# Kernel tuning notes

Measured on AMD Instinct MI355X. Metric: run time of the kernel, lower is better.

Reference implementation:

```python
import jax, jax.numpy as jnp
import numpy as np
from jax import lax

B, CIN, H, W = 8, 64, 128, 128
COUT, K, STRIDE, PAD = 128, 3, 1, 1
NLEV = 256  # 2**activation_bits == 2**weight_bits


def setup_inputs() -> dict:
    key = jax.random.key(0)
    kx, kw = jax.random.split(key)
    x = jax.random.uniform(kx, (B, CIN, H, W), dtype=jnp.float32)
    weight = jax.random.normal(kw, (COUT, CIN, K, K), dtype=jnp.float32)
    bias = jnp.zeros((COUT,), dtype=jnp.float32)
    return {"x": x, "weight": weight, "bias": bias}


def _lut_table(weight):
    # quantized weights in [0, 255], integer-valued
    qw = jnp.clip(jnp.round(weight * (NLEV - 1)), 0, NLEV - 1).astype(jnp.int32)
    iv = jnp.arange(NLEV, dtype=jnp.int32)
    # emulate torch .to(int16) wraparound (qw*i can exceed 32767)
    lut = (qw[..., None] * iv).astype(jnp.int16)          # [O, C, K, K, 256]
    # the original sums pcilt over its (c,p,q) dims for EVERY patch entry;
    # precollapse those dims: T[i, o] = sum_{c,p,q} lut[o,c,p,q,i]
    T = lut.astype(jnp.int32).sum(axis=(1, 2, 3))          # [O, 256]
    return T.T                                             # [256, O]


def reference(x, weight, bias):
    T = _lut_table(weight)                                 # [256, COUT]
    xq = jnp.clip(jnp.round(x * (NLEV - 1)), 0, NLEV - 1).astype(jnp.int32)
    xp = jnp.pad(xq, ((0, 0), (0, 0), (PAD, PAD), (PAD, PAD)))  # zero-pad; T[:,0]=0 matches
    xc = jnp.moveaxis(xp, 1, 0)                            # [CIN, B, Hp, Wp]

    # accumulate per-pixel channel sum of LUT rows: A[b,h,w,o] = sum_c T[x[b,c,h,w], o]
    A0 = jnp.zeros((xp.shape[0], xp.shape[2], xp.shape[3], COUT), dtype=jnp.int32)

    def body(acc, ch):
        return acc + T[ch], None

    A, _ = lax.scan(body, A0, xc)                          # [B, Hp, Wp, COUT]

    # k x k sliding-window sum over spatial dims = sum over all patch entries
    out = lax.reduce_window(A.astype(jnp.float32), 0.0, lax.add,
                            (1, K, K, 1), (1, STRIDE, STRIDE, 1), 'VALID')
    out = jnp.moveaxis(out, 3, 1) + bias[None, :, None, None]  # [B, COUT, OH, OW]
    return out
```

## Files before the change

### kernel.cpp

```cpp
#include <hip/hip_runtime.h>

#define CIN   64
#define HW    128
#define COUT  128
#define TH    8
#define TW    32
#define NITER 12
#define NTHR  512
#define HSTR  144
#define SLOT  (34 * HSTR)
#define H3SL  (32 * HSTR)

#define HM_OFF    0
#define H3_OFF    19584
#define SX_OFF    38016
#define SXP_OFF   39296
#define SX9_OFF   42560
#define LDS_BYTES 42880

typedef int v4i __attribute__((ext_vector_type(4)));

__device__ __forceinline__ void wg_barrier() {
  asm volatile("s_waitcnt lgkmcnt(0)\n\ts_barrier" ::: "memory");
}

__device__ __forceinline__ int quad_sum(int v) {
  v += __builtin_amdgcn_mov_dpp(v, 0xB1, 0xF, 0xF, true);
  v += __builtin_amdgcn_mov_dpp(v, 0x4E, 0xF, 0xF, true);
  return v;
}

__global__ __launch_bounds__(512)
void build_tables(const float* __restrict__ weight, int* __restrict__ W_tab,
                  char* __restrict__ Kt_g) {
  __shared__ int qw_s[576];
  __shared__ int red_s[144];
  const int o = blockIdx.x;
  const int t = threadIdx.x;
  for (int j = t; j < 576; j += 512) {
    float w = weight[o * 576 + j];
    int q = (int)rintf(w * 255.f);
    qw_s[j] = q < 0 ? 0 : (q > 255 ? 255 : q);
  }
  __syncthreads();
  const int v = t >> 2, part = t & 3;
  const int i = 128 + v;
  int cnt = 0;
  const int j0 = part * 144;
  for (int j = j0; j < j0 + 144; ++j) cnt += (qw_s[j] * i) > 32767 ? 1 : 0;
  cnt = quad_sum(cnt);
  if (part == 0) Kt_g[o * 128 + v] = (char)(cnt - 128);
  if (t < 144)
    red_s[t] = qw_s[t * 4] + qw_s[t * 4 + 1] + qw_s[t * 4 + 2] + qw_s[t * 4 + 3];
  __syncthreads();
  if (t == 0) {
    int s = 0;
    for (int kk = 0; kk < 144; ++kk) s += red_s[kk];
    W_tab[o] = s;
  }
}

__global__ __launch_bounds__(NTHR, 4)
void pcilt_main(const float* __restrict__ x, const float* __restrict__ bias,
                const int* __restrict__ W_tab, const char* __restrict__ Kt_g,
                float* __restrict__ out) {
  __shared__ uint4 ldsv[LDS_BYTES / 16];
  char* ldsb = (char*)ldsv;
  unsigned char* HmB = (unsigned char*)(ldsb + HM_OFF);
  unsigned char* H3B = (unsigned char*)(ldsb + H3_OFF);
  unsigned char* KtB = (unsigned char*)(ldsb + H3_OFF);
  int* Sx  = (int*)(ldsb + SX_OFF);
  int* Sxp = (int*)(ldsb + SXP_OFF);
  int* Sx9 = (int*)(ldsb + SX9_OFF);

  const int t   = (int)threadIdx.x;
  const int bid = (int)blockIdx.x;
  const int b  = bid & 7;
  const int k  = bid >> 3;
  const int h0 = (k >> 2) * TH;
  const int w0 = (k & 3) * TW;

  for (int i = t; i < 4096; i += NTHR)
    ((unsigned int*)KtB)[i] = ((const unsigned int*)Kt_g)[i];
  {
    const uint4 z4 = make_uint4(0, 0, 0, 0);
    for (int i = t; i < SLOT / 16; i += NTHR) ((uint4*)HmB)[i] = z4;
  }

  const int l    = t & 15;
  const int slot = t >> 4;
  const int wv   = t >> 6;
  const int kq   = (t >> 4) & 3;
  const int Mt   = wv >> 2;
  const int Nh   = wv & 3;
  const int o0   = Nh * 32 + l;

  const float wfo0 = (float)W_tab[o0],      bio0 = bias[o0];
  const float wfo1 = (float)W_tab[o0 + 16], bio1 = bias[o0 + 16];

  float pf0[4], pf1[4];
  int qv[2][8];
  const float* xb = x + ((size_t)b * CIN + l * 4) * (HW * HW);
  const size_t cs = (size_t)HW * HW;

#define ISSUE(rn)                                                              \
  {                                                                            \
    const int iy  = h0 + (rn)-1;                                               \
    const int iyc = iy < 0 ? 0 : (iy > 127 ? 127 : iy);                        \
    const bool rok = (iy >= 0) && (iy < HW);                                   \
    int ix = w0 + slot - 1;                                                    \
    int ixc = ix < 0 ? 0 : (ix > 127 ? 127 : ix);                              \
    bool ok = rok && (ix >= 0) && (ix < HW);                                   \
    const float* xp = xb + (size_t)iyc * HW + ixc;                             \
    float v0 = xp[0], v1 = xp[cs], v2 = xp[2 * cs], v3 = xp[3 * cs];           \
    pf0[0] = ok ? v0 : 0.f; pf0[1] = ok ? v1 : 0.f;                            \
    pf0[2] = ok ? v2 : 0.f; pf0[3] = ok ? v3 : 0.f;                            \
    if (slot >= 30) {                                                          \
      ix = w0 + slot + 1;                                    \
      ixc = ix > 127 ? 127 : ix;                                               \
      ok = rok && (ix < HW);                                                   \
      const float* xq = xb + (size_t)iyc * HW + ixc;                           \
      float u0 = xq[0], u1 = xq[cs], u2 = xq[2 * cs], u3 = xq[3 * cs];         \
      pf1[0] = ok ? u0 : 0.f; pf1[1] = ok ? u1 : 0.f;                          \
      pf1[2] = ok ? u2 : 0.f; pf1[3] = ok ? u3 : 0.f;                          \
    }                                                                          \
  }

#define QUANT4(pf, qn, base, px, sxpb)                                         \
  {                                                                            \
    int q;                                                                     \
    q = (int)rintf((pf)[0] * 255.f); (qn)[(base)+0] = q < 0 ? 0 : (q > 255 ? 255 : q); \
    q = (int)rintf((pf)[1] * 255.f); (qn)[(base)+1] = q < 0 ? 0 : (q > 255 ? 255 : q); \
    q = (int)rintf((pf)[2] * 255.f); (qn)[(base)+2] = q < 0 ? 0 : (q > 255 ? 255 : q); \
    q = (int)rintf((pf)[3] * 255.f); (qn)[(base)+3] = q < 0 ? 0 : (q > 255 ? 255 : q); \
    int pk = (((qn)[(base)+0] > 128) + ((qn)[(base)+1] > 128) +                \
              ((qn)[(base)+2] > 128) + ((qn)[(base)+3] > 128));                \
    pk = (pk << 20) + (qn)[(base)+0] + (qn)[(base)+1] + (qn)[(base)+2] + (qn)[(base)+3]; \
    pk = quad_sum(pk);                                                         \
    if ((l & 3) == 0) Sxp[(sxpb) + (px)*12 + (l >> 2)] = pk;                   \
  }

#define HIST4(q0, q1, q2, q3, px, Hc)                                          \
  {                                                                            \
    unsigned char* hp = (Hc) + (px)*HSTR;                                      \
    if ((q0) > 128) { int v = (q0) - 128; atomicAdd((unsigned int*)(hp + ((v >> 2) << 2)), 1u << ((v & 3) * 8)); } \
    if ((q1) > 128) { int v = (q1) - 128; atomicAdd((unsigned int*)(hp + ((v >> 2) << 2)), 1u << ((v & 3) * 8)); } \
    if ((q2) > 128) { int v = (q2) - 128; atomicAdd((unsigned int*)(hp + ((v >> 2) << 2)), 1u << ((v & 3) * 8)); } \
    if ((q3) > 128) { int v = (q3) - 128; atomicAdd((unsigned int*)(hp + ((v >> 2) << 2)), 1u << ((v & 3) * 8)); } \
  }

  ISSUE(0);
  wg_barrier();

  v4i bfr[2][2];
#pragma unroll
  for (int nt = 0; nt < 2; ++nt)
#pragma unroll
    for (int k64 = 0; k64 < 2; ++k64)
      bfr[nt][k64] = *(const v4i*)(KtB + (o0 + nt * 16) * 128 + k64 * 64 + kq * 16);

  QUANT4(pf0, qv[0], 0, slot, 0);
  if (slot >= 30) QUANT4(pf1, qv[0], 4, slot + 2, 0);
  ISSUE(1);
  wg_barrier();

#pragma unroll
  for (int r = 0; r < NITER; ++r) {
    if (r <= 9) {
      unsigned char* Hc = HmB + (r & 3) * SLOT;
      const int* qc = qv[r & 1];
      HIST4(qc[0], qc[1], qc[2], qc[3], slot, Hc);
      if (slot >= 30) HIST4(qc[4], qc[5], qc[6], qc[7], slot + 2, Hc);
    }
    if (r >= 1 && r <= 10 && t < 256) {
      const int px = t & 31, ch = (t >> 5) * 16;
      const unsigned char* hs = HmB + ((r - 1) & 3) * SLOT + px * HSTR + ch;
      const uint4 a0 = *(const uint4*)hs;
      const uint4 a1 = *(const uint4*)(hs + HSTR);
      const uint4 a2 = *(const uint4*)(hs + 2 * HSTR);
      uint4 s;
      s.x = a0.x + a1.x + a2.x; s.y = a0.y + a1.y + a2.y;
      s.z = a0.z + a1.z + a2.z; s.w = a0.w + a1.w + a2.w;
      *(uint4*)(H3B + ((r - 1) & 3) * H3SL + px * HSTR + ch) = s;
    }
    if (r >= 4) {
      v4i acc0 = (v4i){0, 0, 0, 0}, acc1 = (v4i){0, 0, 0, 0};
#pragma unroll
      for (int st = 0; st < 3; ++st) {
        const unsigned char* Hs = H3B + ((r - 4 + st) & 3) * H3SL +
                                  (Mt * 16 + l) * HSTR + kq * 16;
#pragma unroll
        for (int k64 = 0; k64 < 2; ++k64) {
          const v4i a = *(const v4i*)(Hs + k64 * 64);
          acc0 = __builtin_amdgcn_mfma_i32_16x16x64_i8(a, bfr[0][k64], acc0, 0, 0, 0);
          acc1 = __builtin_amdgcn_mfma_i32_16x16x64_i8(a, bfr[1][k64], acc1, 0, 0, 0);
        }
      }
      const int j = r - 4, h = h0 + j, px0 = Mt * 16 + kq * 4;
      const v4i s9 = *(const v4i*)&Sx9[(j & 1) * 40 + px0];
      float4 u0, u1;
#pragma unroll
      for (int rg = 0; rg < 4; ++rg) {
        const int sx = s9[rg] & 0xFFFFF;
        const int sh = s9[rg] >> 20;
        ((float*)&u0)[rg] = (float)sx * wfo0 - 65536.f * (float)(acc0[rg] + (sh << 7)) + bio0;
        ((float*)&u1)[rg] = (float)sx * wfo1 - 65536.f * (float)(acc1[rg] + (sh << 7)) + bio1;
      }
      float* op = out + (((size_t)b * COUT + o0) * HW + h) * HW + w0 + px0;
      *(float4*)op = u0;
      *(float4*)(op + 16 * (size_t)(HW * HW)) = u1;
    }
    if (r <= 9 && wv == 7) {
      const int L = t - 448;
      if (L < 34) {
        const v4i sq = *(const v4i*)&Sxp[(r & 1) * 408 + L * 12];
        Sx[(r & 7) * 40 + L] = sq.x + sq.y + sq.z + sq.w;
      }
    }
    if (r >= 3 && r <= 10 && wv == 6 && (t & 32)) {
      const int L = t - 416;
      int v9 = 0;
#pragma unroll
      for (int q = 0; q < 3; ++q) {
        const int sl = ((r - 3 + q) & 7) * 40;
        v9 += Sx[sl + L] + Sx[sl + L + 1] + Sx[sl + L + 2];
      }
      Sx9[((r - 3) & 1) * 40 + L] = v9;
    }
    if (r <= 8 && wv >= 4 && wv < 6) {
      uint4* Hn = (uint4*)(HmB + ((r + 1) & 3) * SLOT);
      const uint4 z4 = make_uint4(0, 0, 0, 0);
      for (int i2 = t - 256; i2 < SLOT / 16; i2 += 128) Hn[i2] = z4;
    }
    if (r <= 8) {
      const int sxpb = ((r + 1) & 1) * 408;
      int* qn = qv[(r + 1) & 1];
      QUANT4(pf0, qn, 0, slot, sxpb);
      if (slot >= 30) QUANT4(pf1, qn, 4, slot + 2, sxpb);
    }
    if (r <= 7) ISSUE(r + 2);

    wg_barrier();
  }
}

extern "C" void kernel_launch(void* const* d_in, const int* in_sizes, int n_in,
                              void* d_out, int out_size, void* d_ws, size_t ws_size,
                              hipStream_t stream) {
  const float* x      = (const float*)d_in[0];
  const float* weight = (const float*)d_in[1];
  const float* bias   = (const float*)d_in[2];
  float* out = (float*)d_out;

  int*  W_tab = (int*)d_ws;
  char* Kt_g  = (char*)d_ws + 512;

  build_tables<<<128, 512, 0, stream>>>(weight, W_tab, Kt_g);

  pcilt_main<<<512, NTHR, 0, stream>>>(x, bias, W_tab, Kt_g, out);
}
```

Baseline: 44.34 us.

## Preload and quantize all input rows upfront, packing bytes and computing row sums once

Replaces the per-iteration prefetch/quantize pipeline with a single upfront loop that loads all 10 input rows, quantizes them into packed byte registers, and computes per-pixel channel sums with a 16-lane DPP reduction written straight to LDS. The 3x3 window sums are then computed once at iteration zero instead of by dedicated waves inside each pipeline step. This is meant to issue all global loads at once for more memory-level parallelism and to drop per-iteration quantization and Sx bookkeeping. The cost is more live registers (20 packed dwords plus the load burst) and a serialized load phase before histogramming starts, with no overlap against compute.

```diff
diff --git a/kernel.cpp b/kernel.cpp
--- a/kernel.cpp
+++ b/kernel.cpp
@@ -13,10 +13,9 @@
 
 #define HM_OFF    0
 #define H3_OFF    19584
-#define SX_OFF    38016
-#define SXP_OFF   39296
-#define SX9_OFF   42560
-#define LDS_BYTES 42880
+#define SXR_OFF   38016
+#define SX9_OFF   39616
+#define LDS_BYTES 40896
 
 typedef int v4i __attribute__((ext_vector_type(4)));
 
@@ -27,6 +26,12 @@
 __device__ __forceinline__ int quad_sum(int v) {
   v += __builtin_amdgcn_mov_dpp(v, 0xB1, 0xF, 0xF, true);
   v += __builtin_amdgcn_mov_dpp(v, 0x4E, 0xF, 0xF, true);
+  return v;
+}
+__device__ __forceinline__ int row16_sum(int v) {
+  v = quad_sum(v);
+  v += __builtin_amdgcn_mov_dpp(v, 0x114, 0xF, 0xF, true);
+  v += __builtin_amdgcn_mov_dpp(v, 0x118, 0xF, 0xF, true);
   return v;
 }
 
@@ -69,8 +74,7 @@
   unsigned char* HmB = (unsigned char*)(ldsb + HM_OFF);
   unsigned char* H3B = (unsigned char*)(ldsb + H3_OFF);
   unsigned char* KtB = (unsigned char*)(ldsb + H3_OFF);
-  int* Sx  = (int*)(ldsb + SX_OFF);
-  int* Sxp = (int*)(ldsb + SXP_OFF);
+  int* SxR = (int*)(ldsb + SXR_OFF);
   int* Sx9 = (int*)(ldsb + SX9_OFF);
 
   const int t   = (int)threadIdx.x;
@@ -98,79 +102,92 @@
   const float wfo0 = (float)W_tab[o0],      bio0 = bias[o0];
   const float wfo1 = (float)W_tab[o0 + 16], bio1 = bias[o0 + 16];
 
-  float pf0[4], pf1[4];
-  int qv[2][8];
-  const float* xb = x + ((size_t)b * CIN + l * 4) * (HW * HW);
-  const size_t cs = (size_t)HW * HW;
-
-#define ISSUE(rn)                                                              \
-  {                                                                            \
-    const int iy  = h0 + (rn)-1;                                               \
-    const int iyc = iy < 0 ? 0 : (iy > 127 ? 127 : iy);                        \
-    const bool rok = (iy >= 0) && (iy < HW);                                   \
-    int ix = w0 + slot - 1;                                                    \
-    int ixc = ix < 0 ? 0 : (ix > 127 ? 127 : ix);                              \
-    bool ok = rok && (ix >= 0) && (ix < HW);                                   \
-    const float* xp = xb + (size_t)iyc * HW + ixc;                             \
-    float v0 = xp[0], v1 = xp[cs], v2 = xp[2 * cs], v3 = xp[3 * cs];           \
-    pf0[0] = ok ? v0 : 0.f; pf0[1] = ok ? v1 : 0.f;                            \
-    pf0[2] = ok ? v2 : 0.f; pf0[3] = ok ? v3 : 0.f;                            \
-    if (slot >= 30) {                                                          \
-      ix = w0 + slot + 1;                                    \
-      ixc = ix > 127 ? 127 : ix;                                               \
-      ok = rok && (ix < HW);                                                   \
-      const float* xq = xb + (size_t)iyc * HW + ixc;                           \
-      float u0 = xq[0], u1 = xq[cs], u2 = xq[2 * cs], u3 = xq[3 * cs];         \
-      pf1[0] = ok ? u0 : 0.f; pf1[1] = ok ? u1 : 0.f;                          \
-      pf1[2] = ok ? u2 : 0.f; pf1[3] = ok ? u3 : 0.f;                          \
-    }                                                                          \
-  }
-
-#define QUANT4(pf, qn, base, px, sxpb)                                         \
-  {                                                                            \
-    int q;                                                                     \
-    q = (int)rintf((pf)[0] * 255.f); (qn)[(base)+0] = q < 0 ? 0 : (q > 255 ? 255 : q); \
-    q = (int)rintf((pf)[1] * 255.f); (qn)[(base)+1] = q < 0 ? 0 : (q > 255 ? 255 : q); \
-    q = (int)rintf((pf)[2] * 255.f); (qn)[(base)+2] = q < 0 ? 0 : (q > 255 ? 255 : q); \
-    q = (int)rintf((pf)[3] * 255.f); (qn)[(base)+3] = q < 0 ? 0 : (q > 255 ? 255 : q); \
-    int pk = (((qn)[(base)+0] > 128) + ((qn)[(base)+1] > 128) +                \
-              ((qn)[(base)+2] > 128) + ((qn)[(base)+3] > 128));                \
-    pk = (pk << 20) + (qn)[(base)+0] + (qn)[(base)+1] + (qn)[(base)+2] + (qn)[(base)+3]; \
-    pk = quad_sum(pk);                                                         \
-    if ((l & 3) == 0) Sxp[(sxpb) + (px)*12 + (l >> 2)] = pk;                   \
-  }
-
-#define HIST4(q0, q1, q2, q3, px, Hc)                                          \
+  wg_barrier();
+
+  v4i bfr[2][2];
+#pragma unroll
+  for (int nt = 0; nt < 2; ++nt)
+#pragma unroll
+    for (int k64 = 0; k64 < 2; ++k64)
+      bfr[nt][k64] = *(const v4i*)(KtB + (o0 + nt * 16) * 128 + k64 * 64 + kq * 16);
+
+  unsigned int qd[10], qd2[10];
+  {
+    const float* xb = x + ((size_t)b * CIN + l * 4) * (HW * HW);
+    const size_t cs = (size_t)HW * HW;
+    const int ix0 = w0 + slot - 1;
+    const int ix0c = ix0 < 0 ? 0 : (ix0 > 127 ? 127 : ix0);
+    const bool wok0 = (ix0 >= 0) && (ix0 < HW);
+    const int ix1 = w0 + slot + 1;
+    const int ix1c = ix1 > 127 ? 127 : ix1;
+    const bool wok1 = ix1 < HW;
+    const bool dual = slot >= 30;
+#pragma unroll
+    for (int row = 0; row < 10; ++row) {
+      const int iy = h0 + row - 1;
+      const int iyc = iy < 0 ? 0 : (iy > 127 ? 127 : iy);
+      const bool rok = (iy >= 0) && (iy < HW);
+      {
+        const float* xp = xb + (size_t)iyc * HW + ix0c;
+        const bool ok = rok && wok0;
+        float f0 = xp[0], f1 = xp[cs], f2 = xp[2 * cs], f3 = xp[3 * cs];
+        f0 = ok ? f0 : 0.f; f1 = ok ? f1 : 0.f; f2 = ok ? f2 : 0.f; f3 = ok ? f3 : 0.f;
+        int q0 = (int)rintf(f0 * 255.f); q0 = q0 < 0 ? 0 : (q0 > 255 ? 255 : q0);
+        int q1 = (int)rintf(f1 * 255.f); q1 = q1 < 0 ? 0 : (q1 > 255 ? 255 : q1);
+        int q2 = (int)rintf(f2 * 255.f); q2 = q2 < 0 ? 0 : (q2 > 255 ? 255 : q2);
+        int q3 = (int)rintf(f3 * 255.f); q3 = q3 < 0 ? 0 : (q3 > 255 ? 255 : q3);
+        qd[row] = (unsigned)q0 | ((unsigned)q1 << 8) | ((unsigned)q2 << 16) | ((unsigned)q3 << 24);
+        int pk = (((q0 > 128) + (q1 > 128) + (q2 > 128) + (q3 > 128)) << 20) +
+                 (q0 + q1 + q2 + q3);
+        pk = row16_sum(pk);
+        if (l == 15) SxR[row * 40 + slot] = pk;
+      }
+      {
+        const float* xp = xb + (size_t)iyc * HW + ix1c;
+        const bool ok = dual && rok && wok1;
+        float f0 = ok ? xp[0] : 0.f, f1 = ok ? xp[cs] : 0.f;
+        float f2 = ok ? xp[2 * cs] : 0.f, f3 = ok ? xp[3 * cs] : 0.f;
+        int q0 = (int)rintf(f0 * 255.f); q0 = q0 < 0 ? 0 : (q0 > 255 ? 255 : q0);
+        int q1 = (int)rintf(f1 * 255.f); q1 = q1 < 0 ? 0 : (q1 > 255 ? 255 : q1);
+        int q2 = (int)rintf(f2 * 255.f); q2 = q2 < 0 ? 0 : (q2 > 255 ? 255 : q2);
+        int q3 = (int)rintf(f3 * 255.f); q3 = q3 < 0 ? 0 : (q3 > 255 ? 255 : q3);
+        qd2[row] = (unsigned)q0 | ((unsigned)q1 << 8) | ((unsigned)q2 << 16) | ((unsigned)q3 << 24);
+        int pk = (((q0 > 128) + (q1 > 128) + (q2 > 128) + (q3 > 128)) << 20) +
+                 (q0 + q1 + q2 + q3);
+        pk = row16_sum(pk);
+        if (dual && l == 15) SxR[row * 40 + slot + 2] = pk;
+      }
+    }
+  }
+  wg_barrier();
+
+#define HISTD(dw, px, Hc)                                                      \
   {                                                                            \
     unsigned char* hp = (Hc) + (px)*HSTR;                                      \
-    if ((q0) > 128) { int v = (q0) - 128; atomicAdd((unsigned int*)(hp + ((v >> 2) << 2)), 1u << ((v & 3) * 8)); } \
-    if ((q1) > 128) { int v = (q1) - 128; atomicAdd((unsigned int*)(hp + ((v >> 2) << 2)), 1u << ((v & 3) * 8)); } \
-    if ((q2) > 128) { int v = (q2) - 128; atomicAdd((unsigned int*)(hp + ((v >> 2) << 2)), 1u << ((v & 3) * 8)); } \
-    if ((q3) > 128) { int v = (q3) - 128; atomicAdd((unsigned int*)(hp + ((v >> 2) << 2)), 1u << ((v & 3) * 8)); } \
-  }
-
-  ISSUE(0);
-  wg_barrier();
-
-  v4i bfr[2][2];
-#pragma unroll
-  for (int nt = 0; nt < 2; ++nt)
-#pragma unroll
-    for (int k64 = 0; k64 < 2; ++k64)
-      bfr[nt][k64] = *(const v4i*)(KtB + (o0 + nt * 16) * 128 + k64 * 64 + kq * 16);
-
-  QUANT4(pf0, qv[0], 0, slot, 0);
-  if (slot >= 30) QUANT4(pf1, qv[0], 4, slot + 2, 0);
-  ISSUE(1);
-  wg_barrier();
+    const unsigned b0 = (dw) & 255u, b1 = ((dw) >> 8) & 255u;                  \
+    const unsigned b2 = ((dw) >> 16) & 255u, b3 = (dw) >> 24;                  \
+    if (b0 > 128u) { unsigned v = b0 - 128u; atomicAdd((unsigned*)(hp + ((v >> 2) << 2)), 1u << ((v & 3) * 8)); } \
+    if (b1 > 128u) { unsigned v = b1 - 128u; atomicAdd((unsigned*)(hp + ((v >> 2) << 2)), 1u << ((v & 3) * 8)); } \
+    if (b2 > 128u) { unsigned v = b2 - 128u; atomicAdd((unsigned*)(hp + ((v >> 2) << 2)), 1u << ((v & 3) * 8)); } \
+    if (b3 > 128u) { unsigned v = b3 - 128u; atomicAdd((unsigned*)(hp + ((v >> 2) << 2)), 1u << ((v & 3) * 8)); } \
+  }
 
 #pragma unroll
   for (int r = 0; r < NITER; ++r) {
     if (r <= 9) {
       unsigned char* Hc = HmB + (r & 3) * SLOT;
-      const int* qc = qv[r & 1];
-      HIST4(qc[0], qc[1], qc[2], qc[3], slot, Hc);
-      if (slot >= 30) HIST4(qc[4], qc[5], qc[6], qc[7], slot + 2, Hc);
+      HISTD(qd[r], slot, Hc);
+      if (slot >= 30) HISTD(qd2[r], slot + 2, Hc);
+    }
+    if (r == 0 && t < 256) {
+      const int j = t >> 5, L = t & 31;
+      int v9 = 0;
+#pragma unroll
+      for (int q = 0; q < 3; ++q) {
+        const int* sr = &SxR[(j + q) * 40 + L];
+        v9 += sr[0] + sr[1] + sr[2];
+      }
+      Sx9[j * 40 + L] = v9;
     }
     if (r >= 1 && r <= 10 && t < 256) {
       const int px = t & 31, ch = (t >> 5) * 16;
@@ -197,7 +214,7 @@
         }
       }
       const int j = r - 4, h = h0 + j, px0 = Mt * 16 + kq * 4;
-      const v4i s9 = *(const v4i*)&Sx9[(j & 1) * 40 + px0];
+      const v4i s9 = *(const v4i*)&Sx9[j * 40 + px0];
       float4 u0, u1;
 #pragma unroll
       for (int rg = 0; rg < 4; ++rg) {
@@ -210,36 +227,11 @@
       *(float4*)op = u0;
       *(float4*)(op + 16 * (size_t)(HW * HW)) = u1;
     }
-    if (r <= 9 && wv == 7) {
-      const int L = t - 448;
-      if (L < 34) {
-        const v4i sq = *(const v4i*)&Sxp[(r & 1) * 408 + L * 12];
-        Sx[(r & 7) * 40 + L] = sq.x + sq.y + sq.z + sq.w;
-      }
-    }
-    if (r >= 3 && r <= 10 && wv == 6 && (t & 32)) {
-      const int L = t - 416;
-      int v9 = 0;
-#pragma unroll
-      for (int q = 0; q < 3; ++q) {
-        const int sl = ((r - 3 + q) & 7) * 40;
-        v9 += Sx[sl + L] + Sx[sl + L + 1] + Sx[sl + L + 2];
-      }
-      Sx9[((r - 3) & 1) * 40 + L] = v9;
-    }
     if (r <= 8 && wv >= 4 && wv < 6) {
       uint4* Hn = (uint4*)(HmB + ((r + 1) & 3) * SLOT);
       const uint4 z4 = make_uint4(0, 0, 0, 0);
       for (int i2 = t - 256; i2 < SLOT / 16; i2 += 128) Hn[i2] = z4;
     }
-    if (r <= 8) {
-      const int sxpb = ((r + 1) & 1) * 408;
-      int* qn = qv[(r + 1) & 1];
-      QUANT4(pf0, qn, 0, slot, sxpb);
-      if (slot >= 30) QUANT4(pf1, qn, 4, slot + 2, sxpb);
-    }
-    if (r <= 7) ISSUE(r + 2);
-
     wg_barrier();
   }
 }
```

Result: slower. 48.97 us (+10.4%).
